# Performance work log

Measured on AMD Instinct MI355X. Metric: run time of the kernel, lower is better.

The kernel has to match this reference:

```python
import jax, jax.numpy as jnp
import numpy as np

N = 1_000_000
D_MODEL = 128
D_PRIN = 64        # d_principle: truncated projected dims used in traversal stage
R = 32             # nsw32 -> fixed out-degree
B = 128            # query batch
E = 32             # random32 entry points
EF = 64            # ef_search (beam width)
K = 10
N_ITERS = 8        # fixed number of beam-expansion rounds (jit-friendly traversal)


def setup_inputs() -> dict:
    key = jax.random.key(0)
    k1, k2, k3, k4, k5 = jax.random.split(key, 5)
    query = jax.random.normal(k1, (B, D_MODEL), jnp.float32)
    VT = jax.random.normal(k2, (D_MODEL, D_MODEL), jnp.float32) / jnp.sqrt(D_MODEL)
    storage = jax.random.normal(k3, (N, D_MODEL), jnp.float32)
    neighbors = jax.random.randint(k4, (N, R), 0, N, jnp.int32)
    entry_ids = jax.random.randint(k5, (E,), 0, N, jnp.int32)
    return {"query": query, "VT": VT, "storage": storage,
            "neighbors": neighbors, "entry_ids": entry_ids,
            "k": K, "ef_search": EF}


def _search(query, VT, storage, neighbors, entry_ids, k, ef_search):
    n = storage.shape[0]
    bq = query.shape[0]
    BIG = jnp.float32(1e30)

    # stage 0: project query into SVD basis; principle dims for traversal
    q_full = query @ VT.T                      # [B, d_model]
    q_p = q_full[:, :D_PRIN]                   # [B, d_p]
    storage_p = storage[:, :D_PRIN]            # [N, d_p]
    sq_p = jnp.sum(storage_p * storage_p, axis=-1)          # [N]
    qn = jnp.sum(q_p * q_p, axis=-1, keepdims=True)         # [B, 1]

    def dist_p(ids):  # squared L2 in principle dims, sentinel id >= n -> BIG
        c = jnp.clip(ids, 0, n - 1)
        d = sq_p[c] - 2.0 * jnp.einsum('bmd,bd->bm', storage_p[c], q_p) + qn
        return jnp.where(ids >= n, BIG, d)

    def dedup_topk(ids, dists, m):
        # sort by id, mask duplicate ids (same id -> same dist), keep best m
        order = jnp.argsort(ids, axis=-1)
        sid = jnp.take_along_axis(ids, order, axis=-1)
        sd = jnp.take_along_axis(dists, order, axis=-1)
        dup = jnp.concatenate(
            [jnp.zeros_like(sid[:, :1], dtype=bool), sid[:, 1:] == sid[:, :-1]], axis=-1)
        sd = jnp.where(dup | (sid >= n), BIG, sd)
        neg, idx = jax.lax.top_k(-sd, m)
        return jnp.take_along_axis(sid, idx, axis=-1), -neg

    # entry stage (random32): distances to fixed entry points
    ids0 = jnp.broadcast_to(entry_ids[None, :], (bq, entry_ids.shape[0]))
    d0 = dist_p(ids0)
    pad = ef_search - ids0.shape[1]
    beam_I = jnp.concatenate([ids0, jnp.full((bq, pad), n, dtype=ids0.dtype)], axis=-1)
    beam_D = jnp.concatenate([d0, jnp.full((bq, pad), BIG, dtype=d0.dtype)], axis=-1)
    beam_I, beam_D = dedup_topk(beam_I, beam_D, ef_search)

    # beam traversal over NSW neighbor lists (principle-dim distances)
    def step(carry, _):
        bI, bD = carry
        nbr = neighbors[jnp.clip(bI, 0, n - 1)]              # [B, ef, R]
        cand = jnp.where(bI[:, :, None] >= n, n, nbr).reshape(bq, -1)
        cD = dist_p(cand)
        aI = jnp.concatenate([bI, cand.astype(bI.dtype)], axis=-1)
        aD = jnp.concatenate([bD, cD], axis=-1)
        return dedup_topk(aI, aD, ef_search), None

    (beam_I, beam_D), _ = jax.lax.scan(step, (beam_I, beam_D), None, length=N_ITERS)

    # final stage: rerank beam with full-dimensional distances, return top-k
    vecs = storage[jnp.clip(beam_I, 0, n - 1)]               # [B, ef, d_model]
    diff = vecs - q_full[:, None, :]
    d_full = jnp.where(beam_I >= n, BIG, jnp.sum(diff * diff, axis=-1))
    neg, idx = jax.lax.top_k(-d_full, k)
    out_I = jnp.take_along_axis(beam_I, idx, axis=-1)
    return out_I, -neg


def reference(query, VT, storage, neighbors, entry_ids, k, ef_search):
    return _search(query, VT, storage, neighbors, entry_ids, k, ef_search)
```

## Files before the change

kernel.cpp:

```cpp
#include <hip/hip_runtime.h>

typedef unsigned long long ull;

#define N_PTS   1000000
#define DM      128
#define DP      64
#define RNB     32
#define ENT     32
#define EFS     64
#define KOUT    10
#define N_ITERS 8
#define NTH     512
#define NWAVE   (NTH / 64)
#define HASHCAP 32768
#define MAXNEW  2112
#define BIGF    1e30f
#define PADKEY  0xFFFFFFFFFFFFFFFFull

__device__ __forceinline__ unsigned fkey_enc(float d) {
  unsigned b = __float_as_uint(d);
  return (b & 0x80000000u) ? ~b : (b | 0x80000000u);
}

__device__ __forceinline__ float dist_p(const float* __restrict__ storage,
                                        const float* qf, float qn, int id) {
  int c = id < 0 ? 0 : (id > N_PTS - 1 ? N_PTS - 1 : id);
  const float4* row = (const float4*)(storage + (size_t)c * DM);
  float sq = 0.f, dt = 0.f;
#pragma unroll
  for (int j = 0; j < DP / 4; ++j) {
    float4 s = row[j];
    sq = fmaf(s.x, s.x, sq); sq = fmaf(s.y, s.y, sq);
    sq = fmaf(s.z, s.z, sq); sq = fmaf(s.w, s.w, sq);
    dt = fmaf(s.x, qf[4*j+0], dt); dt = fmaf(s.y, qf[4*j+1], dt);
    dt = fmaf(s.z, qf[4*j+2], dt); dt = fmaf(s.w, qf[4*j+3], dt);
  }
  float d = sq - 2.f * dt + qn;
  return (id >= N_PTS) ? BIGF : d;
}

__device__ __forceinline__ bool visit_claim(int* htab, int id) {
  unsigned h = ((unsigned)id * 2654435761u) & (HASHCAP - 1);
  while (true) {
    int cur = htab[h];
    if (cur == id) return false;
    if (cur == -1) {
      int old = atomicCAS(&htab[h], -1, id);
      if (old == -1) return true;
      if (old == id) return false;
    }
    h = (h + 1) & (HASHCAP - 1);
  }
}

__device__ __forceinline__ ull wsort64(ull key, int lane) {
#pragma unroll
  for (int k = 2; k <= 64; k <<= 1) {
#pragma unroll
    for (int j = k >> 1; j > 0; j >>= 1) {
      ull other = __shfl_xor(key, j);
      bool up = ((lane & k) == 0);
      bool lower = ((lane & j) == 0);
      ull mn = key < other ? key : other;
      ull mx = key < other ? other : key;
      key = (up == lower) ? mn : mx;
    }
  }
  return key;
}

__device__ __forceinline__ ull wbmerge64(ull key, int lane) {
#pragma unroll
  for (int j = 32; j > 0; j >>= 1) {
    ull other = __shfl_xor(key, j);
    bool lower = ((lane & j) == 0);
    ull mn = key < other ? key : other;
    ull mx = key < other ? other : key;
    key = lower ? mn : mx;
  }
  return key;
}

__device__ __forceinline__ ull wmerge(ull a, ull b, int lane) {
  ull brev = __shfl_xor(b, 63);
  ull c = a < brev ? a : brev;
  return wbmerge64(c, lane);
}

__global__ __launch_bounds__(NTH) void search_kernel(
    const float* __restrict__ query,
    const float* __restrict__ VT,
    const float* __restrict__ storage,
    const int*   __restrict__ neighbors,
    const int*   __restrict__ entry_ids,
    float* __restrict__ out)
{
  __shared__ int   htab[HASHCAP];
  __shared__ ull   newkeys[MAXNEW];
  __shared__ ull   wavetop[NWAVE + 4][64];
  __shared__ ull   beamkey[EFS];
  __shared__ int   beam_id[EFS];
  __shared__ float qf[DM];
  __shared__ float qloc[DM];
  __shared__ float qn_s;
  __shared__ int   nc;
  __shared__ float dfull[EFS];

  const int b    = blockIdx.x;
  const int B    = gridDim.x;
  const int tid  = threadIdx.x;
  const int lane = tid & 63;
  const int wid  = tid >> 6;

  const ull FILLKEY = ((ull)fkey_enc(BIGF) << 32) | (unsigned)N_PTS;

  for (int i = tid; i < HASHCAP; i += NTH) htab[i] = -1;

  if (tid < DM) qloc[tid] = query[(size_t)b * DM + tid];
  __syncthreads();
  if (tid < DM) {
    const float* vrow = VT + (size_t)tid * DM;
    float acc = 0.f;
#pragma unroll 8
    for (int d = 0; d < DM; ++d) acc = fmaf(qloc[d], vrow[d], acc);
    qf[tid] = acc;
  }
  __syncthreads();
  if (tid == 0) {
    float acc = 0.f;
    for (int d = 0; d < DP; ++d) acc = fmaf(qf[d], qf[d], acc);
    qn_s = acc;
  }
  __syncthreads();
  const float qn = qn_s;

  if (wid == 0) {
    ull ek = PADKEY;
    if (lane < ENT) {
      int id = entry_ids[lane];
      if (visit_claim(htab, id)) {
        float d = dist_p(storage, qf, qn, id);
        ek = ((ull)fkey_enc(d) << 32) | (unsigned)id;
      }
    }
    ek = wsort64(ek, lane);
    if (ek == PADKEY) ek = FILLKEY;
    beamkey[lane] = ek;
    beam_id[lane] = (int)(ek & 0xFFFFFFFFull);
  }
  __syncthreads();

  for (int it = 0; it < N_ITERS; ++it) {
    ull kmax = beamkey[EFS - 1];
    if (tid == 0) nc = 0;
    __syncthreads();

    for (int ci = tid; ci < EFS * RNB; ci += NTH) {
      int e = ci >> 5;
      int r = ci & 31;
      int bid = beam_id[e];
      if (bid >= N_PTS) continue;
      int cid = neighbors[(size_t)bid * RNB + r];
      if (!visit_claim(htab, cid)) continue;
      float d = dist_p(storage, qf, qn, cid);
      ull key = ((ull)fkey_enc(d) << 32) | (unsigned)cid;
      if (key < kmax) {
        int p = atomicAdd(&nc, 1);
        newkeys[p] = key;
      }
    }
    __syncthreads();

    int cnt = nc;
    if (cnt == 0) break;

    ull t = PADKEY;
    int nchunks = (cnt + 63) >> 6;
    for (int c = wid; c < nchunks; c += NWAVE) {
      int idx = (c << 6) + lane;
      ull v = (idx < cnt) ? newkeys[idx] : PADKEY;
      v = wsort64(v, lane);
      t = wmerge(t, v, lane);
    }
    wavetop[wid][lane] = t;
    __syncthreads();

    if (wid < 4) {
      ull a = wavetop[2 * wid][lane];
      ull bb = wavetop[2 * wid + 1][lane];
      wavetop[NWAVE + wid][lane] = wmerge(a, bb, lane);
    }
    __syncthreads();
    if (wid == 0) {
      ull m0 = wmerge(wavetop[NWAVE + 0][lane], wavetop[NWAVE + 1][lane], lane);
      ull m1 = wmerge(wavetop[NWAVE + 2][lane], wavetop[NWAVE + 3][lane], lane);
      ull t2 = wmerge(m0, m1, lane);
      ull nb = wmerge(beamkey[lane], t2, lane);
      beamkey[lane] = nb;
      beam_id[lane] = (int)(nb & 0xFFFFFFFFull);
    }
    __syncthreads();
  }

  if (wid == 0) {
    int id = beam_id[lane];
    int c = id < 0 ? 0 : (id > N_PTS - 1 ? N_PTS - 1 : id);
    const float4* row = (const float4*)(storage + (size_t)c * DM);
    float acc = 0.f;
#pragma unroll
    for (int j = 0; j < DM / 4; ++j) {
      float4 s = row[j];
      float dx = s.x - qf[4*j+0]; acc = fmaf(dx, dx, acc);
      dx = s.y - qf[4*j+1]; acc = fmaf(dx, dx, acc);
      dx = s.z - qf[4*j+2]; acc = fmaf(dx, dx, acc);
      dx = s.w - qf[4*j+3]; acc = fmaf(dx, dx, acc);
    }
    float dv = (id >= N_PTS) ? BIGF : acc;
    dfull[lane] = dv;
    ull fk = ((ull)fkey_enc(dv) << 32) | (unsigned)lane;
    fk = wsort64(fk, lane);
    if (lane < KOUT) {
      int pos = (int)(fk & 0xFFFFFFFFull);
      out[(size_t)b * KOUT + lane] = (float)beam_id[pos];
      out[(size_t)B * KOUT + (size_t)b * KOUT + lane] = dfull[pos];
    }
  }
}

extern "C" void kernel_launch(void* const* d_in, const int* in_sizes, int n_in,
                              void* d_out, int out_size, void* d_ws, size_t ws_size,
                              hipStream_t stream) {
  const float* query     = (const float*)d_in[0];
  const float* VT        = (const float*)d_in[1];
  const float* storage   = (const float*)d_in[2];
  const int*   neighbors = (const int*)d_in[3];
  const int*   entry_ids = (const int*)d_in[4];
  float* out = (float*)d_out;

  int B = in_sizes[0] / DM;
  search_kernel<<<B, NTH, 0, stream>>>(query, VT, storage, neighbors, entry_ids, out);
}
```

Measured before the change: 113.1 us.

## Split claim and distance phases, compact candidates, double block threads

The candidate loop is split into two phases. First, neighbor ids are claimed in the hash table and compacted into a shared list using wave-aggregated atomics. Second, distances are computed over the dense list, so no lanes sit idle on duplicate or already-visited ids. The block size doubles to 1024 threads, giving more loads in flight per query, and the merge tree gains a level to fold 16 wave tops. The cost is an extra barrier per iteration and lower occupancy headroom; only 128 blocks run in total.

```diff
diff --git a/kernel.cpp b/kernel.cpp
--- a/kernel.cpp
+++ b/kernel.cpp
@@ -10,10 +10,10 @@
 #define EFS     64
 #define KOUT    10
 #define N_ITERS 8
-#define NTH     512
+#define NTH     1024
 #define NWAVE   (NTH / 64)
 #define HASHCAP 32768
-#define MAXNEW  2112
+#define MAXNEW  2048
 #define BIGF    1e30f
 #define PADKEY  0xFFFFFFFFFFFFFFFFull
 
@@ -85,6 +85,19 @@
   ull brev = __shfl_xor(b, 63);
   ull c = a < brev ? a : brev;
   return wbmerge64(c, lane);
+}
+
+__device__ __forceinline__ int wave_append(int* counter, bool want, int lane) {
+  ull mask = __ballot(want);
+  int pos = -1;
+  if (mask) {
+    int leader = __ffsll((long long)mask) - 1;
+    int base = 0;
+    if (lane == leader) base = atomicAdd(counter, (int)__popcll(mask));
+    base = __shfl(base, leader);
+    pos = base + (int)__popcll(mask & ((1ull << lane) - 1ull));
+  }
+  return pos;
 }
 
 __global__ __launch_bounds__(NTH) void search_kernel(
@@ -97,14 +110,16 @@
 {
   __shared__ int   htab[HASHCAP];
   __shared__ ull   newkeys[MAXNEW];
-  __shared__ ull   wavetop[NWAVE + 4][64];
+  __shared__ ull   scratch[NWAVE * 64];
   __shared__ ull   beamkey[EFS];
   __shared__ int   beam_id[EFS];
   __shared__ float qf[DM];
   __shared__ float qloc[DM];
   __shared__ float qn_s;
-  __shared__ int   nc;
+  __shared__ int   nclaim, nc;
   __shared__ float dfull[EFS];
+
+  int* evalids = (int*)scratch;
 
   const int b    = blockIdx.x;
   const int B    = gridDim.x;
@@ -152,49 +167,71 @@
 
   for (int it = 0; it < N_ITERS; ++it) {
     ull kmax = beamkey[EFS - 1];
-    if (tid == 0) nc = 0;
-    __syncthreads();
-
+    if (tid == 0) { nclaim = 0; nc = 0; }
+    __syncthreads();
+
+#pragma unroll
     for (int ci = tid; ci < EFS * RNB; ci += NTH) {
       int e = ci >> 5;
       int r = ci & 31;
       int bid = beam_id[e];
-      if (bid >= N_PTS) continue;
-      int cid = neighbors[(size_t)bid * RNB + r];
-      if (!visit_claim(htab, cid)) continue;
+      bool want = false;
+      int cid = 0;
+      if (bid < N_PTS) {
+        cid = neighbors[(size_t)bid * RNB + r];
+        want = visit_claim(htab, cid);
+      }
+      int pos = wave_append(&nclaim, want, lane);
+      if (want) evalids[pos] = cid;
+    }
+    __syncthreads();
+
+    int ne = nclaim;
+    int ntrips = (ne + NTH - 1) / NTH;
+    for (int t = 0; t < ntrips; ++t) {
+      int i = t * NTH + tid;
+      bool valid = i < ne;
+      int cid = valid ? evalids[i] : 0;
       float d = dist_p(storage, qf, qn, cid);
       ull key = ((ull)fkey_enc(d) << 32) | (unsigned)cid;
-      if (key < kmax) {
-        int p = atomicAdd(&nc, 1);
-        newkeys[p] = key;
-      }
+      bool pass = valid && (key < kmax);
+      int pos = wave_append(&nc, pass, lane);
+      if (pass) newkeys[pos] = key;
     }
     __syncthreads();
 
     int cnt = nc;
     if (cnt == 0) break;
 
-    ull t = PADKEY;
+    ull tk = PADKEY;
     int nchunks = (cnt + 63) >> 6;
     for (int c = wid; c < nchunks; c += NWAVE) {
       int idx = (c << 6) + lane;
       ull v = (idx < cnt) ? newkeys[idx] : PADKEY;
       v = wsort64(v, lane);
-      t = wmerge(t, v, lane);
-    }
-    wavetop[wid][lane] = t;
-    __syncthreads();
-
-    if (wid < 4) {
-      ull a = wavetop[2 * wid][lane];
-      ull bb = wavetop[2 * wid + 1][lane];
-      wavetop[NWAVE + wid][lane] = wmerge(a, bb, lane);
-    }
+      tk = wmerge(tk, v, lane);
+    }
+    __syncthreads();
+    scratch[wid * 64 + lane] = tk;
+    __syncthreads();
+
+    ull m8 = PADKEY;
+    if (wid < 8) {
+      ull a  = scratch[(2 * wid) * 64 + lane];
+      ull bb = scratch[(2 * wid + 1) * 64 + lane];
+      m8 = wmerge(a, bb, lane);
+    }
+    __syncthreads();
+    if (wid < 8) scratch[wid * 64 + lane] = m8;
     __syncthreads();
     if (wid == 0) {
-      ull m0 = wmerge(wavetop[NWAVE + 0][lane], wavetop[NWAVE + 1][lane], lane);
-      ull m1 = wmerge(wavetop[NWAVE + 2][lane], wavetop[NWAVE + 3][lane], lane);
-      ull t2 = wmerge(m0, m1, lane);
+      ull m0 = wmerge(scratch[0 * 64 + lane], scratch[1 * 64 + lane], lane);
+      ull m1 = wmerge(scratch[2 * 64 + lane], scratch[3 * 64 + lane], lane);
+      ull m2 = wmerge(scratch[4 * 64 + lane], scratch[5 * 64 + lane], lane);
+      ull m3 = wmerge(scratch[6 * 64 + lane], scratch[7 * 64 + lane], lane);
+      ull t0 = wmerge(m0, m1, lane);
+      ull t1 = wmerge(m2, m3, lane);
+      ull t2 = wmerge(t0, t1, lane);
       ull nb = wmerge(beamkey[lane], t2, lane);
       beamkey[lane] = nb;
       beam_id[lane] = (int)(nb & 0xFFFFFFFFull);
```

Measured after the change: 130.2 us. +15.1%, slower.

## Split each query across two cooperating blocks by candidate-id parity

Applied to the files above, without the earlier changes.

Launches two blocks per query as a cooperative kernel. Each block evaluates only the candidates whose id has its parity, then the pair exchange their per-iteration top-64 through global memory with flag spin-waits and merge the results. Both blocks also stop early once the beam no longer changes. This doubles the blocks working on the distance gathers, at the cost of a global handshake every iteration, a flag memset, and duplicated hash-table and qf setup in both blocks. It falls back to the single-block kernel when workspace or cooperative launch is unavailable.

```diff
diff --git a/kernel.cpp b/kernel.cpp
--- a/kernel.cpp
+++ b/kernel.cpp
@@ -9,7 +9,7 @@
 #define ENT     32
 #define EFS     64
 #define KOUT    10
-#define N_ITERS 8
+#define NITERS  8
 #define NTH     512
 #define NWAVE   (NTH / 64)
 #define HASHCAP 32768
@@ -87,13 +87,189 @@
   return wbmerge64(c, lane);
 }
 
-__global__ __launch_bounds__(NTH) void search_kernel(
-    const float* __restrict__ query,
-    const float* __restrict__ VT,
-    const float* __restrict__ storage,
-    const int*   __restrict__ neighbors,
-    const int*   __restrict__ entry_ids,
-    float* __restrict__ out)
+
+__device__ __forceinline__ void compute_qf(const float* query, const float* VT,
+                                           float* qloc, float* qf, float* qn_s,
+                                           int b, int tid) {
+  if (tid < DM) qloc[tid] = query[(size_t)b * DM + tid];
+  __syncthreads();
+  if (tid < DM) {
+    const float* vrow = VT + (size_t)tid * DM;
+    float acc = 0.f;
+#pragma unroll 8
+    for (int d = 0; d < DM; ++d) acc = fmaf(qloc[d], vrow[d], acc);
+    qf[tid] = acc;
+  }
+  __syncthreads();
+  if (tid == 0) {
+    float acc = 0.f;
+    for (int d = 0; d < DP; ++d) acc = fmaf(qf[d], qf[d], acc);
+    *qn_s = acc;
+  }
+  __syncthreads();
+}
+
+__device__ __forceinline__ void final_topk(const float* storage, const float* qf,
+                                           const int* beam_id, float* dfull,
+                                           float* out, int b, int B,
+                                           int lane, int wid) {
+  if (wid == 0) {
+    int id = beam_id[lane];
+    int c = id < 0 ? 0 : (id > N_PTS - 1 ? N_PTS - 1 : id);
+    const float4* row = (const float4*)(storage + (size_t)c * DM);
+    float acc = 0.f;
+#pragma unroll
+    for (int j = 0; j < DM / 4; ++j) {
+      float4 s = row[j];
+      float dx = s.x - qf[4*j+0]; acc = fmaf(dx, dx, acc);
+      dx = s.y - qf[4*j+1]; acc = fmaf(dx, dx, acc);
+      dx = s.z - qf[4*j+2]; acc = fmaf(dx, dx, acc);
+      dx = s.w - qf[4*j+3]; acc = fmaf(dx, dx, acc);
+    }
+    float dv = (id >= N_PTS) ? BIGF : acc;
+    dfull[lane] = dv;
+    ull fk = ((ull)fkey_enc(dv) << 32) | (unsigned)lane;
+    fk = wsort64(fk, lane);
+    if (lane < KOUT) {
+      int pos = (int)(fk & 0xFFFFFFFFull);
+      out[(size_t)b * KOUT + lane] = (float)beam_id[pos];
+      out[(size_t)B * KOUT + (size_t)b * KOUT + lane] = dfull[pos];
+    }
+  }
+}
+
+
+__global__ __launch_bounds__(NTH) void search_pair(
+    const float* __restrict__ query, const float* __restrict__ VT,
+    const float* __restrict__ storage, const int* __restrict__ neighbors,
+    const int* __restrict__ entry_ids, float* __restrict__ out,
+    ull* __restrict__ pay,
+    int* __restrict__ flags,
+    int B)
+{
+  __shared__ int   htab[HASHCAP];
+  __shared__ ull   newkeys[MAXNEW];
+  __shared__ ull   wavetop[NWAVE][64];
+  __shared__ ull   beamkey[EFS];
+  __shared__ int   beam_id[EFS];
+  __shared__ float qf[DM];
+  __shared__ float qloc[DM];
+  __shared__ float qn_s;
+  __shared__ int   nc, stop;
+  __shared__ float dfull[EFS];
+
+  const int pair   = blockIdx.x >> 1;
+  const int parity = blockIdx.x & 1;
+  const int b      = pair;
+  const int tid    = threadIdx.x;
+  const int lane   = tid & 63;
+  const int wid    = tid >> 6;
+
+  const ull FILLKEY = ((ull)fkey_enc(BIGF) << 32) | (unsigned)N_PTS;
+
+  for (int i = tid; i < HASHCAP; i += NTH) htab[i] = -1;
+
+  compute_qf(query, VT, qloc, qf, &qn_s, b, tid);
+  const float qn = qn_s;
+
+  if (wid == 0) {
+    ull ek = PADKEY;
+    if (lane < ENT) {
+      int id = entry_ids[lane];
+      if (visit_claim(htab, id)) {
+        float d = dist_p(storage, qf, qn, id);
+        ek = ((ull)fkey_enc(d) << 32) | (unsigned)id;
+      }
+    }
+    ek = wsort64(ek, lane);
+    if (ek == PADKEY) ek = FILLKEY;
+    beamkey[lane] = ek;
+    beam_id[lane] = (int)(ek & 0xFFFFFFFFull);
+  }
+  __syncthreads();
+
+  for (int it = 0; it < NITERS; ++it) {
+    ull kmax = beamkey[EFS - 1];
+    if (tid == 0) nc = 0;
+    __syncthreads();
+
+    for (int ci = tid; ci < EFS * RNB; ci += NTH) {
+      int e = ci >> 5;
+      int r = ci & 31;
+      int bid = beam_id[e];
+      if (bid >= N_PTS) continue;
+      int cid = neighbors[(size_t)bid * RNB + r];
+      if (!visit_claim(htab, cid)) continue;
+      if ((cid & 1) != parity) continue;
+      float d = dist_p(storage, qf, qn, cid);
+      ull key = ((ull)fkey_enc(d) << 32) | (unsigned)cid;
+      if (key < kmax) {
+        int p = atomicAdd(&nc, 1);
+        newkeys[p] = key;
+      }
+    }
+    __syncthreads();
+
+    int cnt = nc;
+
+    ull tk = PADKEY;
+    int nchunks = (cnt + 63) >> 6;
+    for (int c = wid; c < nchunks; c += NWAVE) {
+      int idx = (c << 6) + lane;
+      ull v = (idx < cnt) ? newkeys[idx] : PADKEY;
+      v = wsort64(v, lane);
+      tk = wmerge(tk, v, lane);
+    }
+    wavetop[wid][lane] = tk;
+    __syncthreads();
+
+    ull* slot_my = pay + (((size_t)pair * NITERS + it) * 2 + parity) * 64;
+    ull* slot_pt = pay + (((size_t)pair * NITERS + it) * 2 + (parity ^ 1)) * 64;
+    int* flag_my = flags + (((size_t)pair * NITERS + it) * 2 + parity);
+    int* flag_pt = flags + (((size_t)pair * NITERS + it) * 2 + (parity ^ 1));
+
+    if (wid == 0) {
+      ull m0 = wmerge(wavetop[0][lane], wavetop[1][lane], lane);
+      ull m1 = wmerge(wavetop[2][lane], wavetop[3][lane], lane);
+      ull m2 = wmerge(wavetop[4][lane], wavetop[5][lane], lane);
+      ull m3 = wmerge(wavetop[6][lane], wavetop[7][lane], lane);
+      ull t0 = wmerge(m0, m1, lane);
+      ull t1 = wmerge(m2, m3, lane);
+      ull mytop = wmerge(t0, t1, lane);
+      wavetop[0][lane] = mytop;
+      slot_my[lane] = mytop;
+      __threadfence();
+    }
+    __syncthreads();
+    if (tid == 0) {
+      atomicExch(flag_my, 1);
+      while (atomicCAS(flag_pt, 1, 1) == 0) __builtin_amdgcn_s_sleep(8);
+    }
+    __syncthreads();
+
+    if (wid == 0) {
+      __threadfence();
+      ull ptop = slot_pt[lane];
+      ull t2 = wmerge(wavetop[0][lane], ptop, lane);
+      ull old = beamkey[lane];
+      ull nb = wmerge(old, t2, lane);
+      ull same = __ballot(nb == old);
+      beamkey[lane] = nb;
+      beam_id[lane] = (int)(nb & 0xFFFFFFFFull);
+      if (lane == 0) stop = (same == ~0ull) ? 1 : 0;
+    }
+    __syncthreads();
+    if (stop) break;
+  }
+
+  if (parity == 0) final_topk(storage, qf, beam_id, dfull, out, b, B, lane, wid);
+}
+
+
+__global__ __launch_bounds__(NTH) void search_solo(
+    const float* __restrict__ query, const float* __restrict__ VT,
+    const float* __restrict__ storage, const int* __restrict__ neighbors,
+    const int* __restrict__ entry_ids, float* __restrict__ out)
 {
   __shared__ int   htab[HASHCAP];
   __shared__ ull   newkeys[MAXNEW];
@@ -116,22 +292,7 @@
 
   for (int i = tid; i < HASHCAP; i += NTH) htab[i] = -1;
 
-  if (tid < DM) qloc[tid] = query[(size_t)b * DM + tid];
-  __syncthreads();
-  if (tid < DM) {
-    const float* vrow = VT + (size_t)tid * DM;
-    float acc = 0.f;
-#pragma unroll 8
-    for (int d = 0; d < DM; ++d) acc = fmaf(qloc[d], vrow[d], acc);
-    qf[tid] = acc;
-  }
-  __syncthreads();
-  if (tid == 0) {
-    float acc = 0.f;
-    for (int d = 0; d < DP; ++d) acc = fmaf(qf[d], qf[d], acc);
-    qn_s = acc;
-  }
-  __syncthreads();
+  compute_qf(query, VT, qloc, qf, &qn_s, b, tid);
   const float qn = qn_s;
 
   if (wid == 0) {
@@ -150,7 +311,7 @@
   }
   __syncthreads();
 
-  for (int it = 0; it < N_ITERS; ++it) {
+  for (int it = 0; it < NITERS; ++it) {
     ull kmax = beamkey[EFS - 1];
     if (tid == 0) nc = 0;
     __syncthreads();
@@ -202,29 +363,7 @@
     __syncthreads();
   }
 
-  if (wid == 0) {
-    int id = beam_id[lane];
-    int c = id < 0 ? 0 : (id > N_PTS - 1 ? N_PTS - 1 : id);
-    const float4* row = (const float4*)(storage + (size_t)c * DM);
-    float acc = 0.f;
-#pragma unroll
-    for (int j = 0; j < DM / 4; ++j) {
-      float4 s = row[j];
-      float dx = s.x - qf[4*j+0]; acc = fmaf(dx, dx, acc);
-      dx = s.y - qf[4*j+1]; acc = fmaf(dx, dx, acc);
-      dx = s.z - qf[4*j+2]; acc = fmaf(dx, dx, acc);
-      dx = s.w - qf[4*j+3]; acc = fmaf(dx, dx, acc);
-    }
-    float dv = (id >= N_PTS) ? BIGF : acc;
-    dfull[lane] = dv;
-    ull fk = ((ull)fkey_enc(dv) << 32) | (unsigned)lane;
-    fk = wsort64(fk, lane);
-    if (lane < KOUT) {
-      int pos = (int)(fk & 0xFFFFFFFFull);
-      out[(size_t)b * KOUT + lane] = (float)beam_id[pos];
-      out[(size_t)B * KOUT + (size_t)b * KOUT + lane] = dfull[pos];
-    }
-  }
+  final_topk(storage, qf, beam_id, dfull, out, b, B, lane, wid);
 }
 
 extern "C" void kernel_launch(void* const* d_in, const int* in_sizes, int n_in,
@@ -238,5 +377,21 @@
   float* out = (float*)d_out;
 
   int B = in_sizes[0] / DM;
-  search_kernel<<<B, NTH, 0, stream>>>(query, VT, storage, neighbors, entry_ids, out);
-}
+
+  size_t pay_bytes  = (size_t)B * NITERS * 2 * 64 * sizeof(ull);
+  size_t flag_bytes = (size_t)B * NITERS * 2 * sizeof(int);
+
+  if (ws_size >= pay_bytes + flag_bytes) {
+    ull* pay   = (ull*)d_ws;
+    int* flags = (int*)((char*)d_ws + pay_bytes);
+    hipMemsetAsync(flags, 0, flag_bytes, stream);
+    void* args[] = {(void*)&query, (void*)&VT, (void*)&storage, (void*)&neighbors,
+                    (void*)&entry_ids, (void*)&out, (void*)&pay, (void*)&flags,
+                    (void*)&B};
+    hipError_t e = hipLaunchCooperativeKernel((const void*)search_pair,
+                                              dim3(2 * B), dim3(NTH),
+                                              args, 0, stream);
+    if (e == hipSuccess) return;
+  }
+  search_solo<<<B, NTH, 0, stream>>>(query, VT, storage, neighbors, entry_ids, out);
+}
```

After: 171.6 us. +51.6%, slower.

## Software-pipeline candidate row loads with double-buffered registers and query in registers

Applied to the files above, without the earlier changes.

The candidate distance loop is restructured so each thread first gathers all four neighbor ids, then loads storage rows into two register buffers, overlapping the next row's gather with the current row's distance computation. The query vector is held in registers rather than read from shared memory. Distances are now computed before the visited-set check, so already-visited candidates are still loaded and evaluated, which adds memory traffic. The 128 extra float4 registers per thread at 512 threads may also limit occupancy or cause spills.

```diff
diff --git a/kernel.cpp b/kernel.cpp
--- a/kernel.cpp
+++ b/kernel.cpp
@@ -9,7 +9,7 @@
 #define ENT     32
 #define EFS     64
 #define KOUT    10
-#define N_ITERS 8
+#define NITERS  8
 #define NTH     512
 #define NWAVE   (NTH / 64)
 #define HASHCAP 32768
@@ -86,6 +86,33 @@
   ull c = a < brev ? a : brev;
   return wbmerge64(c, lane);
 }
+
+#define LOAD_ROW(BUF, K)                                                  \
+  {                                                                       \
+    int cc_ = cids[K]; cc_ = cc_ < N_PTS ? cc_ : 0;                       \
+    const float4* row_ = (const float4*)(storage + (size_t)cc_ * DM);     \
+    _Pragma("unroll")                                                     \
+    for (int j = 0; j < 16; ++j) BUF[j] = row_[j];                        \
+  }
+
+#define EVAL_ROW(BUF, K)                                                  \
+  {                                                                       \
+    float sq_ = 0.f, dt_ = 0.f;                                           \
+    _Pragma("unroll")                                                     \
+    for (int j = 0; j < 16; ++j) {                                        \
+      float4 s_ = BUF[j];                                                 \
+      sq_ = fmaf(s_.x, s_.x, sq_); sq_ = fmaf(s_.y, s_.y, sq_);           \
+      sq_ = fmaf(s_.z, s_.z, sq_); sq_ = fmaf(s_.w, s_.w, sq_);           \
+      dt_ = fmaf(s_.x, qreg[j].x, dt_); dt_ = fmaf(s_.y, qreg[j].y, dt_); \
+      dt_ = fmaf(s_.z, qreg[j].z, dt_); dt_ = fmaf(s_.w, qreg[j].w, dt_); \
+    }                                                                     \
+    float d_ = sq_ - 2.f * dt_ + qn;                                      \
+    int cid_ = cids[K];                                                   \
+    if (cid_ < N_PTS && visit_claim(htab, cid_)) {                        \
+      ull key_ = ((ull)fkey_enc(d_) << 32) | (unsigned)cid_;              \
+      if (key_ < kmax) { int p_ = atomicAdd(&nc, 1); newkeys[p_] = key_; }\
+    }                                                                     \
+  }
 
 __global__ __launch_bounds__(NTH) void search_kernel(
     const float* __restrict__ query,
@@ -100,7 +127,7 @@
   __shared__ ull   wavetop[NWAVE + 4][64];
   __shared__ ull   beamkey[EFS];
   __shared__ int   beam_id[EFS];
-  __shared__ float qf[DM];
+  __shared__ __align__(16) float qf[DM];
   __shared__ float qloc[DM];
   __shared__ float qn_s;
   __shared__ int   nc;
@@ -133,6 +160,10 @@
   }
   __syncthreads();
   const float qn = qn_s;
+
+  float4 qreg[16];
+#pragma unroll
+  for (int j = 0; j < 16; ++j) qreg[j] = ((const float4*)qf)[j];
 
   if (wid == 0) {
     ull ek = PADKEY;
@@ -150,39 +181,44 @@
   }
   __syncthreads();
 
-  for (int it = 0; it < N_ITERS; ++it) {
+  for (int it = 0; it < NITERS; ++it) {
     ull kmax = beamkey[EFS - 1];
     if (tid == 0) nc = 0;
     __syncthreads();
 
-    for (int ci = tid; ci < EFS * RNB; ci += NTH) {
-      int e = ci >> 5;
-      int r = ci & 31;
-      int bid = beam_id[e];
-      if (bid >= N_PTS) continue;
-      int cid = neighbors[(size_t)bid * RNB + r];
-      if (!visit_claim(htab, cid)) continue;
-      float d = dist_p(storage, qf, qn, cid);
-      ull key = ((ull)fkey_enc(d) << 32) | (unsigned)cid;
-      if (key < kmax) {
-        int p = atomicAdd(&nc, 1);
-        newkeys[p] = key;
+    {
+      int cids[4];
+#pragma unroll
+      for (int k = 0; k < 4; ++k) {
+        int ci = tid + k * NTH;
+        int bid = beam_id[ci >> 5];
+        cids[k] = (bid < N_PTS) ? neighbors[(size_t)bid * RNB + (ci & 31)]
+                                : N_PTS;
       }
+      float4 bufA[16], bufB[16];
+      LOAD_ROW(bufA, 0)
+      LOAD_ROW(bufB, 1)
+      EVAL_ROW(bufA, 0)
+      LOAD_ROW(bufA, 2)
+      EVAL_ROW(bufB, 1)
+      LOAD_ROW(bufB, 3)
+      EVAL_ROW(bufA, 2)
+      EVAL_ROW(bufB, 3)
     }
     __syncthreads();
 
     int cnt = nc;
     if (cnt == 0) break;
 
-    ull t = PADKEY;
+    ull tk = PADKEY;
     int nchunks = (cnt + 63) >> 6;
     for (int c = wid; c < nchunks; c += NWAVE) {
       int idx = (c << 6) + lane;
       ull v = (idx < cnt) ? newkeys[idx] : PADKEY;
       v = wsort64(v, lane);
-      t = wmerge(t, v, lane);
-    }
-    wavetop[wid][lane] = t;
+      tk = wmerge(tk, v, lane);
+    }
+    wavetop[wid][lane] = tk;
     __syncthreads();
 
     if (wid < 4) {
```

Result: slower. 173.0 us (+52.9%).
